# Kernel tuning notes

Measured on AMD Instinct MI355X. Metric: run time of the kernel, lower is better.

## Reference

```python
import jax, jax.numpy as jnp
import numpy as np

D_MODEL = 1024
N_HEAD = 16
D_K = D_MODEL // N_HEAD
MAX_LEN = 1000
LN_EPS = 1e-5


def setup_inputs() -> dict:
    key = jax.random.key(0)
    ks = jax.random.split(key, 12)
    B, S = 4, 1000
    def xavier(k, shape):
        fan_in, fan_out = shape[1], shape[0]
        lim = np.sqrt(6.0 / (fan_in + fan_out))
        return jax.random.uniform(k, shape, jnp.float32, -lim, lim)
    return {
        "q": jax.random.normal(ks[0], (B, S, D_MODEL), jnp.float32),
        "k": jax.random.normal(ks[1], (B, S, D_MODEL), jnp.float32),
        "v": jax.random.normal(ks[2], (B, S, D_MODEL), jnp.float32),
        "ln_g": jnp.ones((D_MODEL,), jnp.float32),
        "ln_b": jnp.zeros((D_MODEL,), jnp.float32),
        "wq": xavier(ks[3], (D_MODEL, D_MODEL)),
        "bq": jnp.zeros((D_MODEL,), jnp.float32),
        "wk": xavier(ks[4], (D_MODEL, D_MODEL)),
        "bk": jnp.zeros((D_MODEL,), jnp.float32),
        "wv": xavier(ks[5], (D_MODEL, D_MODEL)),
        "bv": jnp.zeros((D_MODEL,), jnp.float32),
        "wo": xavier(ks[6], (D_MODEL, D_MODEL)),
        "bo": jnp.zeros((D_MODEL,), jnp.float32),
        "rel_emb": jax.random.normal(ks[7], (2 * MAX_LEN - 1, D_K), jnp.float32) / np.sqrt(D_K),
    }


def _layer_norm(x, g, b):
    mu = jnp.mean(x, axis=-1, keepdims=True)
    var = jnp.mean(jnp.square(x - mu), axis=-1, keepdims=True)
    return (x - mu) * jax.lax.rsqrt(var + LN_EPS) * g + b


def reference(q, k, v, ln_g, ln_b, wq, bq, wk, bk, wv, bv, wo, bo, rel_emb):
    B, S, _ = q.shape
    residual = q
    qn = _layer_norm(q, ln_g, ln_b)
    kn = _layer_norm(k, ln_g, ln_b)
    vn = _layer_norm(v, ln_g, ln_b)
    # torch Linear: y = x @ W^T + b; reshape to [B, H, S, d_k]
    def proj(x, w, b):
        return (x @ w.T + b).reshape(B, S, N_HEAD, D_K).transpose(0, 2, 1, 3)
    qh = proj(qn, wq, bq)
    kh = proj(kn, wk, bk)
    vh = proj(vn, wv, bv)
    scale = 1.0 / np.sqrt(D_K)
    scores = jnp.einsum('bhid,bhjd->bhij', qh, kh) * scale
    # relative position bias: rel_pos[i, j] = emb[center + (i - j)]
    center = MAX_LEN - 1
    start = center - (S - 1)
    window = jax.lax.dynamic_slice_in_dim(rel_emb, start, 2 * S - 1, axis=0)  # [2S-1, d_k]
    pos = jnp.arange(S)
    rel_idx = pos[:, None] - pos[None, :] + (S - 1)  # [S, S] in [0, 2S-2]
    rel_pos = window[rel_idx]  # [S, S, d_k]
    scores = scores + jnp.einsum('bhik,ijk->bhij', qh, rel_pos) * scale
    attn = jax.nn.softmax(scores, axis=-1)
    out = jnp.einsum('bhij,bhjd->bhid', attn, vh)
    out = out.transpose(0, 2, 1, 3).reshape(B, S, D_MODEL)
    out = out @ wo.T + bo
    return out + residual
```

## Files before the change

kernel.cpp:

```cpp
#include <hip/hip_runtime.h>
#include <hip/hip_bf16.h>

#define D_MODEL 1024
#define N_HEAD  16
#define D_K     64
#define MAX_LEN 1000
#define B_      4
#define S_      1000
#define S_PAD   1024
#define M_PAD   (B_ * S_PAD)
#define M_REAL  (B_ * S_)
#define LN_EPS  1e-5f
#define SCALE_L2E 0.1803368801111204f
#define REL_ROWS (2*MAX_LEN-1)

typedef __attribute__((ext_vector_type(8))) short short8;
typedef __attribute__((ext_vector_type(4))) float f32x4;

__device__ __forceinline__ unsigned short f2b(float f) {
    unsigned u = __builtin_bit_cast(unsigned, f);
    u = (u + 0x7FFFu + ((u >> 16) & 1u)) >> 16;
    return (unsigned short)u;
}

__device__ __forceinline__ unsigned short f2b_trunc(float f) {
    return (unsigned short)(__builtin_bit_cast(unsigned, f) >> 16);
}

__device__ __forceinline__ float b2f(unsigned short u) {
    return __builtin_bit_cast(float, (unsigned)u << 16);
}

__device__ __forceinline__ f32x4 mfma16(short8 a, short8 b, f32x4 c) {
    return __builtin_amdgcn_mfma_f32_16x16x32_bf16(a, b, c, 0, 0, 0);
}

__device__ __forceinline__ void gload_lds16(const void* g, void* l) {
    __builtin_amdgcn_global_load_lds(
        (const __attribute__((address_space(1))) unsigned int*)g,
        (__attribute__((address_space(3))) unsigned int*)l, 16, 0, 0);
}

#define DPPROR(x, S) __builtin_bit_cast(float, __builtin_amdgcn_update_dpp( \
        0, __builtin_bit_cast(int, (x)), 0x120 | (S), 0xF, 0xF, false))

__global__ void prep_all(const float* __restrict__ wq, const float* __restrict__ wk,
                         const float* __restrict__ wv, const float* __restrict__ wo,
                         const float* __restrict__ rel,
                         unsigned short* __restrict__ wqb, unsigned short* __restrict__ wkb,
                         unsigned short* __restrict__ wvb, unsigned short* __restrict__ wob,
                         unsigned short* __restrict__ relb,
                         const float* __restrict__ xq, const float* __restrict__ xk,
                         const float* __restrict__ xv, const float* __restrict__ g,
                         const float* __restrict__ beta,
                         unsigned short* __restrict__ yq, unsigned short* __restrict__ yk,
                         unsigned short* __restrict__ yv) {
    __shared__ float rs[4], rq[4];
    int bid = blockIdx.x;
    int tid = threadIdx.x;
    if (bid < 5120) {
        int y = bid >> 10;
        const float* in; unsigned short* out; int n4;
        switch (y) {
            case 0: in = wq; out = wqb; n4 = 262144; break;
            case 1: in = wk; out = wkb; n4 = 262144; break;
            case 2: in = wv; out = wvb; n4 = 262144; break;
            case 3: in = wo; out = wob; n4 = 262144; break;
            default: in = rel; out = relb; n4 = REL_ROWS * D_K / 4; break;
        }
        int i = (bid & 1023) * 256 + tid;
        if (i >= n4) return;
        float4 v = ((const float4*)in)[i];
        ushort4 o;
        o.x = f2b(v.x); o.y = f2b(v.y); o.z = f2b(v.z); o.w = f2b(v.w);
        ((ushort4*)out)[i] = o;
        return;
    }
    int r2 = bid - 5120;
    int which = r2 >> 12;
    int r = r2 & 4095;
    const float* x = which == 0 ? xq : which == 1 ? xk : xv;
    unsigned short* y = which == 0 ? yq : which == 1 ? yk : yv;
    int b = r >> 10, i = r & 1023;
    unsigned short* yr = y + (size_t)r * D_MODEL;
    if (i >= S_) {
#pragma unroll
        for (int l = 0; l < 4; ++l) yr[tid + l * 256] = 0;
        return;
    }
    const float* xr = x + ((size_t)b * S_ + i) * D_MODEL;
    float v[4];
    float s = 0.f, sq = 0.f;
#pragma unroll
    for (int l = 0; l < 4; ++l) {
        v[l] = xr[tid + l * 256];
        s += v[l];
        sq += v[l] * v[l];
    }
#pragma unroll
    for (int o = 32; o > 0; o >>= 1) {
        s += __shfl_down(s, o, 64);
        sq += __shfl_down(sq, o, 64);
    }
    if ((tid & 63) == 0) { rs[tid >> 6] = s; rq[tid >> 6] = sq; }
    __syncthreads();
    if (tid == 0) {
        rs[0] = rs[0] + rs[1] + rs[2] + rs[3];
        rq[0] = rq[0] + rq[1] + rq[2] + rq[3];
    }
    __syncthreads();
    float mu = rs[0] * (1.0f / D_MODEL);
    float var = rq[0] * (1.0f / D_MODEL) - mu * mu;
    float rstd = rsqrtf(var + LN_EPS);
#pragma unroll
    for (int l = 0; l < 4; ++l) {
        int c = tid + l * 256;
        yr[c] = f2b((v[l] - mu) * rstd * g[c] + beta[c]);
    }
}

template<int MODE>
__device__ __forceinline__ void gemm_body(
        const unsigned short* __restrict__ X, const unsigned short* __restrict__ W,
        const float* __restrict__ bias, const float* __restrict__ resid,
        unsigned short* __restrict__ Yb, float* __restrict__ Yf,
        unsigned short* As, unsigned short* Bs, int row0, int col0) {
    int tid = threadIdx.x;
    int lane = tid & 63, w = tid >> 6;
    int wr = w >> 1, wc = w & 1;
    int fr = lane & 15, fk = (lane >> 4) * 8;

    f32x4 acc[4][4];
#pragma unroll
    for (int fm = 0; fm < 4; ++fm)
#pragma unroll
        for (int fn = 0; fn < 4; ++fn) acc[fm][fn] = (f32x4)0.f;

    int c0 = (w * 2 + 0) * 64 + lane;
    int c1 = (w * 2 + 1) * 64 + lane;
    const unsigned short* xs0 = X + (size_t)(row0 + (c0 >> 2)) * 1024 + (c0 & 3) * 8;
    const unsigned short* xs1 = X + (size_t)(row0 + (c1 >> 2)) * 1024 + (c1 & 3) * 8;
    const unsigned short* ws0 = W + (size_t)(col0 + (c0 >> 2)) * 1024 + (c0 & 3) * 8;
    const unsigned short* ws1 = W + (size_t)(col0 + (c1 >> 2)) * 1024 + (c1 & 3) * 8;
    int do0 = (w * 2 + 0) * 512;
    int do1 = (w * 2 + 1) * 512;

    auto stage = [&](int buf, int k0) {
        gload_lds16(xs0 + k0, As + buf * 4096 + do0);
        gload_lds16(xs1 + k0, As + buf * 4096 + do1);
        gload_lds16(ws0 + k0, Bs + buf * 4096 + do0);
        gload_lds16(ws1 + k0, Bs + buf * 4096 + do1);
    };

    stage(0, 0);

    for (int it = 0; it < 32; ++it) {
        __syncthreads();
        if (it < 31) stage((it & 1) ^ 1, (it + 1) * 32);

        const unsigned short* Ab = As + (it & 1) * 4096;
        const unsigned short* Bb = Bs + (it & 1) * 4096;
        short8 a[4], b[4];
#pragma unroll
        for (int fm = 0; fm < 4; ++fm)
            a[fm] = *(const short8*)(Ab + (wr * 64 + fm * 16 + fr) * 32 + fk);
#pragma unroll
        for (int fn = 0; fn < 4; ++fn)
            b[fn] = *(const short8*)(Bb + (wc * 64 + fn * 16 + fr) * 32 + fk);
#pragma unroll
        for (int fm = 0; fm < 4; ++fm)
#pragma unroll
            for (int fn = 0; fn < 4; ++fn)
                acc[fm][fn] = mfma16(a[fm], b[fn], acc[fm][fn]);
    }

#pragma unroll
    for (int fm = 0; fm < 4; ++fm) {
#pragma unroll
        for (int fn = 0; fn < 4; ++fn) {
            int cg = col0 + wc * 64 + fn * 16 + fr;
            float bv = bias[cg];
#pragma unroll
            for (int r = 0; r < 4; ++r) {
                int rg = row0 + wr * 64 + fm * 16 + (lane >> 4) * 4 + r;
                float val = acc[fm][fn][r] + bv;
                int b_ = rg >> 10, i = rg & 1023;
                if (MODE == 0) {
                    int h = cg >> 6, d = cg & 63;
                    Yb[(((size_t)(b_ * N_HEAD + h)) * S_PAD + i) * D_K + d] = f2b(val);
                } else if (MODE == 1) {
                    int h = cg >> 6, d = cg & 63;
                    Yb[(((size_t)(b_ * N_HEAD + h)) * D_K + d) * S_PAD + i] = f2b(val);
                } else {
                    if (i < S_) {
                        size_t orow = (size_t)b_ * S_ + i;
                        Yf[orow * 1024 + cg] = val + resid[orow * 1024 + cg];
                    }
                }
            }
        }
    }
}

__global__ __launch_bounds__(256) void gemm_qkv(
        const unsigned short* __restrict__ qn, const unsigned short* __restrict__ kn,
        const unsigned short* __restrict__ vn,
        const unsigned short* __restrict__ wqb, const unsigned short* __restrict__ wkb,
        const unsigned short* __restrict__ wvb,
        const float* __restrict__ bq, const float* __restrict__ bk,
        const float* __restrict__ bv,
        unsigned short* __restrict__ qh, unsigned short* __restrict__ kh,
        unsigned short* __restrict__ vt) {
    __shared__ __align__(16) unsigned short As[2][128 * 32];
    __shared__ __align__(16) unsigned short Bs[2][128 * 32];
    int fid = blockIdx.x + (blockIdx.y << 3) + (blockIdx.z << 8);
    int swz = (fid & 7) * 96 + (fid >> 3);
    int bz = swz >> 8;
    int rem = swz & 255;
    int row0 = (rem >> 3) * 128, col0 = (rem & 7) * 128;
    if (bz == 0)
        gemm_body<0>(qn, wqb, bq, nullptr, qh, nullptr, As[0], Bs[0], row0, col0);
    else if (bz == 1)
        gemm_body<0>(kn, wkb, bk, nullptr, kh, nullptr, As[0], Bs[0], row0, col0);
    else
        gemm_body<1>(vn, wvb, bv, nullptr, vt, nullptr, As[0], Bs[0], row0, col0);
}

__global__ __launch_bounds__(256) void gemm_out(
        const unsigned short* __restrict__ X, const unsigned short* __restrict__ W,
        const float* __restrict__ bias, const float* __restrict__ resid,
        float* __restrict__ Yf) {
    __shared__ __align__(16) unsigned short As[2][128 * 32];
    __shared__ __align__(16) unsigned short Bs[2][128 * 32];
    int fid = blockIdx.x + (blockIdx.y << 3);
    int swz = (fid & 7) * 32 + (fid >> 3);
    int row0 = (swz >> 3) * 128, col0 = (swz & 7) * 128;
    gemm_body<2>(X, W, bias, resid, nullptr, Yf, As[0], Bs[0], row0, col0);
}

#define QRT 20
#define QPW 1600
#define PW  72
__device__ __forceinline__ void attn_slab(
        const unsigned short* __restrict__ Kc, const unsigned short* __restrict__ Vc,
        unsigned short* __restrict__ qp, const short8 (*rl)[2],
        short8 aq0, short8 aq1, f32x4* accO, float* mrun, float* lrun,
        bool mask_needed, int j0, int fr, int fk8, int rgrp, int rsw) {
    f32x4 accS[4];
#pragma unroll
    for (int fj = 0; fj < 4; ++fj) accS[fj] = (f32x4)0.f;
    __builtin_amdgcn_s_setprio(1);
#pragma unroll
    for (int fj = 0; fj < 4; ++fj) {
        int kb = (fj * 16 + fr) * 64 + fk8;
        accS[fj] = mfma16(aq0, *(const short8*)(Kc + (kb ^ rsw)), accS[fj]);
        accS[fj] = mfma16(aq1, *(const short8*)(Kc + ((kb + 32) ^ rsw)), accS[fj]);
    }
#pragma unroll
    for (int fu = 0; fu < 5; ++fu) {
        f32x4 qr = (f32x4)0.f;
        qr = mfma16(aq0, rl[fu][0], qr);
        qr = mfma16(aq1, rl[fu][1], qr);
        unsigned lo = ((unsigned)f2b_trunc(qr[1]) << 16) | f2b_trunc(qr[0]);
        unsigned hi = ((unsigned)f2b_trunc(qr[3]) << 16) | f2b_trunc(qr[2]);
        *(uint2*)(qp + (fu * 16 + fr) * QRT + rgrp) = uint2{lo, hi};
    }
    __builtin_amdgcn_s_setprio(0);

    float sc[4][4];
#pragma unroll
    for (int fj = 0; fj < 4; ++fj) {
        int j_loc = fj * 16 + fr;
#pragma unroll
        for (int r = 0; r < 4; ++r) {
            int col = rgrp + r - j_loc + 63;
            sc[fj][r] = (accS[fj][r] + b2f(qp[col * QRT + rgrp + r])) * SCALE_L2E;
        }
    }
    if (mask_needed) {
#pragma unroll
        for (int fj = 0; fj < 4; ++fj) {
            int j_loc = fj * 16 + fr;
            if (j0 + j_loc >= S_) {
#pragma unroll
                for (int r = 0; r < 4; ++r) sc[fj][r] = -3e38f;
            }
        }
    }

    float pm[4];
#pragma unroll
    for (int r = 0; r < 4; ++r) {
        float m0 = fmaxf(fmaxf(sc[0][r], sc[1][r]), fmaxf(sc[2][r], sc[3][r]));
        m0 = fmaxf(m0, DPPROR(m0, 1));
        m0 = fmaxf(m0, DPPROR(m0, 2));
        m0 = fmaxf(m0, DPPROR(m0, 4));
        m0 = fmaxf(m0, DPPROR(m0, 8));
        pm[r] = m0;
    }

    float dmax = fmaxf(fmaxf(pm[0] - mrun[0], pm[1] - mrun[1]),
                       fmaxf(pm[2] - mrun[2], pm[3] - mrun[3]));
    if (!__all(dmax <= 8.0f)) {
#pragma unroll
        for (int r = 0; r < 4; ++r) {
            float mn = fmaxf(mrun[r], pm[r]);
            float scl = __builtin_amdgcn_exp2f(mrun[r] - mn);
            mrun[r] = mn;
            lrun[r] *= scl;
#pragma unroll
            for (int fd = 0; fd < 4; ++fd) accO[fd][r] *= scl;
        }
    }

    float rsum[4];
#pragma unroll
    for (int r = 0; r < 4; ++r) rsum[r] = 0.f;
#pragma unroll
    for (int fj = 0; fj < 4; ++fj) {
#pragma unroll
        for (int r = 0; r < 4; ++r) {
            float p = __builtin_amdgcn_exp2f(sc[fj][r] - mrun[r]);
            rsum[r] += p;
            qp[(rgrp + r) * PW + fj * 16 + fr] = f2b_trunc(p);
        }
    }
#pragma unroll
    for (int r = 0; r < 4; ++r) {
        float s0 = rsum[r];
        s0 += DPPROR(s0, 1);
        s0 += DPPROR(s0, 2);
        s0 += DPPROR(s0, 4);
        s0 += DPPROR(s0, 8);
        lrun[r] += s0;
    }

    short8 ap0 = *(const short8*)(qp + fr * PW + fk8);
    short8 ap1 = *(const short8*)(qp + fr * PW + 32 + fk8);
    __builtin_amdgcn_s_setprio(1);
#pragma unroll
    for (int fd = 0; fd < 4; ++fd) {
        int vb = (fd * 16 + fr) * 64 + fk8;
        accO[fd] = mfma16(ap0, *(const short8*)(Vc + (vb ^ rsw)), accO[fd]);
        accO[fd] = mfma16(ap1, *(const short8*)(Vc + ((vb + 32) ^ rsw)), accO[fd]);
    }
    __builtin_amdgcn_s_setprio(0);
}

__global__ __launch_bounds__(256, 2) void attn_mfma(
        const unsigned short* __restrict__ qh, const unsigned short* __restrict__ kh,
        const unsigned short* __restrict__ vt, const unsigned short* __restrict__ relb,
        unsigned short* __restrict__ aout) {
    __shared__ __align__(16) unsigned short Ks[2][64 * 64];
    __shared__ __align__(16) unsigned short Vs[2][64 * 64];
    __shared__ __align__(16) unsigned short QP[8][QPW];

    int tid = threadIdx.x, lane = tid & 63, w = tid >> 6;
    int bid = blockIdx.x;
    int swz = (bid & 7) * 64 + (bid >> 3);
    int bh = swz >> 3;
    int i0a = (((swz & 7) * 8) + 2 * w) * 16;
    int fr = lane & 15, fk8 = (lane >> 4) * 8, rgrp = (lane >> 4) * 4;
    int rsw = (fr & 7) << 3;

    const unsigned short* kbase = kh + (size_t)bh * S_PAD * D_K;
    const unsigned short* vtbase = vt + (size_t)bh * D_K * S_PAD;

    const unsigned short* qpa = qh + ((size_t)bh * S_PAD + i0a + fr) * D_K + fk8;
    short8 aqa0 = *(const short8*)(qpa);
    short8 aqa1 = *(const short8*)(qpa + 32);
    const unsigned short* qpb = qpa + 16 * D_K;
    short8 aqb0 = *(const short8*)(qpb);
    short8 aqb1 = *(const short8*)(qpb + 32);

    f32x4 accOa[4], accOb[4];
    float mruna[4], lruna[4], mrunb[4], lrunb[4];
#pragma unroll
    for (int fd = 0; fd < 4; ++fd) { accOa[fd] = (f32x4)0.f; accOb[fd] = (f32x4)0.f; }
#pragma unroll
    for (int r = 0; r < 4; ++r) {
        mruna[r] = -3e38f; lruna[r] = 0.f;
        mrunb[r] = -3e38f; lrunb[r] = 0.f;
    }

    unsigned short* qpA = QP[w];
    unsigned short* qpB = QP[4 + w];
    int row_in = lane >> 3, slot = lane & 7;

    auto stage = [&](int buf, int it2) {
        int j0s = it2 * 64;
#pragma unroll
        for (int cc = 0; cc < 2; ++cc) {
            int c = w * 2 + cc;
            int r = c * 8 + row_in;
            gload_lds16(kbase + (size_t)(j0s + r) * 64 + (slot ^ row_in) * 8,
                        &Ks[buf][c * 512]);
        }
#pragma unroll
        for (int cc = 0; cc < 2; ++cc) {
            int c = w * 2 + cc;
            int d = c * 8 + row_in;
            gload_lds16(vtbase + (size_t)d * S_PAD + j0s + (slot ^ row_in) * 8,
                        &Vs[buf][c * 512]);
        }
    };

    stage(0, 0);
    __syncthreads();

    for (int it = 0; it < 16; ++it) {
        int cur = it & 1, j0 = it * 64;
        bool mask_needed = (j0 + 63 >= S_);

        short8 rl[6][2];
        int ub = i0a - j0 + (S_ - D_K);
#pragma unroll
        for (int fu = 0; fu < 6; ++fu) {
            int u = ub + fu * 16 + fr;
            u = u < 0 ? 0 : (u > REL_ROWS - 1 ? REL_ROWS - 1 : u);
            const unsigned short* rp = relb + (size_t)u * D_K + fk8;
            rl[fu][0] = *(const short8*)(rp);
            rl[fu][1] = *(const short8*)(rp + 32);
        }
        __builtin_amdgcn_sched_barrier(0);

        if (it < 15) stage(cur ^ 1, it + 1);

        attn_slab(Ks[cur], Vs[cur], qpA, rl, aqa0, aqa1, accOa, mruna, lruna,
                  mask_needed, j0, fr, fk8, rgrp, rsw);
        attn_slab(Ks[cur], Vs[cur], qpB, rl + 1, aqb0, aqb1, accOb, mrunb, lrunb,
                  mask_needed, j0, fr, fk8, rgrp, rsw);

        __syncthreads();
    }

    int b_ = bh >> 4, h = bh & 15;
#pragma unroll
    for (int r = 0; r < 4; ++r) {
        float inva = 1.0f / lruna[r];
        float invb = 1.0f / lrunb[r];
        int ma = b_ * S_PAD + i0a + rgrp + r;
        int mb = ma + 16;
#pragma unroll
        for (int fd = 0; fd < 4; ++fd) {
            int c = h * D_K + fd * 16 + fr;
            aout[(size_t)ma * D_MODEL + c] = f2b(accOa[fd][r] * inva);
            aout[(size_t)mb * D_MODEL + c] = f2b(accOb[fd][r] * invb);
        }
    }
}

extern "C" void kernel_launch(void* const* d_in, const int* in_sizes, int n_in,
                              void* d_out, int out_size, void* d_ws, size_t ws_size,
                              hipStream_t stream) {
    const float* q    = (const float*)d_in[0];
    const float* k    = (const float*)d_in[1];
    const float* v    = (const float*)d_in[2];
    const float* ln_g = (const float*)d_in[3];
    const float* ln_b = (const float*)d_in[4];
    const float* wq   = (const float*)d_in[5];
    const float* bq   = (const float*)d_in[6];
    const float* wk   = (const float*)d_in[7];
    const float* bk   = (const float*)d_in[8];
    const float* wv   = (const float*)d_in[9];
    const float* bv   = (const float*)d_in[10];
    const float* wo   = (const float*)d_in[11];
    const float* bo   = (const float*)d_in[12];
    const float* rel  = (const float*)d_in[13];
    float* out = (float*)d_out;

    const size_t TSZ = (size_t)M_PAD * D_MODEL;
    unsigned short* ws   = (unsigned short*)d_ws;
    unsigned short* qn   = ws;
    unsigned short* kn   = qn + TSZ;
    unsigned short* vn   = kn + TSZ;
    unsigned short* qh   = vn + TSZ;
    unsigned short* kh   = qh + TSZ;
    unsigned short* vt   = kh + TSZ;
    unsigned short* aout = vt + TSZ;
    unsigned short* wqb  = aout + TSZ;
    unsigned short* wkb  = wqb + 1024 * 1024;
    unsigned short* wvb  = wkb + 1024 * 1024;
    unsigned short* wob  = wvb + 1024 * 1024;
    unsigned short* relb = wob + 1024 * 1024;

    prep_all<<<5120 + 3 * 4096, 256, 0, stream>>>(
        wq, wk, wv, wo, rel, wqb, wkb, wvb, wob, relb,
        q, k, v, ln_g, ln_b, qn, kn, vn);

    gemm_qkv<<<dim3(8, 32, 3), 256, 0, stream>>>(qn, kn, vn, wqb, wkb, wvb,
                                                 bq, bk, bv, qh, kh, vt);

    attn_mfma<<<512, 256, 0, stream>>>(qh, kh, vt, relb, aout);

    gemm_out<<<dim3(8, 32), 256, 0, stream>>>(aout, wob, bo, q, out);
}
```

Baseline: 166.0 us.

## Interleave two query slabs per wave and fold softmax scale into Q projection

The two per-wave query slabs, previously processed one after the other, are now handled together in one routine. Each K and V fragment read from LDS feeds both slabs' MFMAs, and the independent softmax chains interleave for more instruction-level parallelism. The softmax scale times log2(e) is now applied once in the Q projection epilogue, which removes the per-score multiply in attention. The cost is higher register pressure under the two-blocks-per-CU launch bound, plus a small precision change because the scaled Q is rounded to bf16.

Result: no change. 163.6 us (median of 2 runs) (-1.4%).

```diff
diff --git a/kernel.cpp b/kernel.cpp
--- a/kernel.cpp
+++ b/kernel.cpp
@@ -185,7 +185,8 @@
                 int rg = row0 + wr * 64 + fm * 16 + (lane >> 4) * 4 + r;
                 float val = acc[fm][fn][r] + bv;
                 int b_ = rg >> 10, i = rg & 1023;
-                if (MODE == 0) {
+                if (MODE == 0 || MODE == 3) {
+                    if (MODE == 3) val *= SCALE_L2E;
                     int h = cg >> 6, d = cg & 63;
                     Yb[(((size_t)(b_ * N_HEAD + h)) * S_PAD + i) * D_K + d] = f2b(val);
                 } else if (MODE == 1) {
@@ -219,7 +220,7 @@
     int rem = swz & 255;
     int row0 = (rem >> 3) * 128, col0 = (rem & 7) * 128;
     if (bz == 0)
-        gemm_body<0>(qn, wqb, bq, nullptr, qh, nullptr, As[0], Bs[0], row0, col0);
+        gemm_body<3>(qn, wqb, bq, nullptr, qh, nullptr, As[0], Bs[0], row0, col0);
     else if (bz == 1)
         gemm_body<0>(kn, wkb, bk, nullptr, kh, nullptr, As[0], Bs[0], row0, col0);
     else
@@ -241,40 +242,57 @@
 #define QRT 20
 #define QPW 1600
 #define PW  72
-__device__ __forceinline__ void attn_slab(
+__device__ __forceinline__ void attn_pair(
         const unsigned short* __restrict__ Kc, const unsigned short* __restrict__ Vc,
-        unsigned short* __restrict__ qp, const short8 (*rl)[2],
-        short8 aq0, short8 aq1, f32x4* accO, float* mrun, float* lrun,
+        unsigned short* __restrict__ qpA, unsigned short* __restrict__ qpB,
+        const short8 (*rl)[2],
+        short8 aqa0, short8 aqa1, short8 aqb0, short8 aqb1,
+        f32x4* accOa, f32x4* accOb,
+        float* mra, float* lra, float* mrb, float* lrb,
         bool mask_needed, int j0, int fr, int fk8, int rgrp, int rsw) {
-    f32x4 accS[4];
-#pragma unroll
-    for (int fj = 0; fj < 4; ++fj) accS[fj] = (f32x4)0.f;
+    f32x4 accS0[4], accS1[4];
+#pragma unroll
+    for (int fj = 0; fj < 4; ++fj) { accS0[fj] = (f32x4)0.f; accS1[fj] = (f32x4)0.f; }
     __builtin_amdgcn_s_setprio(1);
 #pragma unroll
     for (int fj = 0; fj < 4; ++fj) {
         int kb = (fj * 16 + fr) * 64 + fk8;
-        accS[fj] = mfma16(aq0, *(const short8*)(Kc + (kb ^ rsw)), accS[fj]);
-        accS[fj] = mfma16(aq1, *(const short8*)(Kc + ((kb + 32) ^ rsw)), accS[fj]);
+        short8 kf0 = *(const short8*)(Kc + (kb ^ rsw));
+        short8 kf1 = *(const short8*)(Kc + ((kb + 32) ^ rsw));
+        accS0[fj] = mfma16(aqa0, kf0, accS0[fj]);
+        accS1[fj] = mfma16(aqb0, kf0, accS1[fj]);
+        accS0[fj] = mfma16(aqa1, kf1, accS0[fj]);
+        accS1[fj] = mfma16(aqb1, kf1, accS1[fj]);
     }
 #pragma unroll
     for (int fu = 0; fu < 5; ++fu) {
         f32x4 qr = (f32x4)0.f;
-        qr = mfma16(aq0, rl[fu][0], qr);
-        qr = mfma16(aq1, rl[fu][1], qr);
+        qr = mfma16(aqa0, rl[fu][0], qr);
+        qr = mfma16(aqa1, rl[fu][1], qr);
         unsigned lo = ((unsigned)f2b_trunc(qr[1]) << 16) | f2b_trunc(qr[0]);
         unsigned hi = ((unsigned)f2b_trunc(qr[3]) << 16) | f2b_trunc(qr[2]);
-        *(uint2*)(qp + (fu * 16 + fr) * QRT + rgrp) = uint2{lo, hi};
+        *(uint2*)(qpA + (fu * 16 + fr) * QRT + rgrp) = uint2{lo, hi};
+    }
+#pragma unroll
+    for (int fu = 0; fu < 5; ++fu) {
+        f32x4 qr = (f32x4)0.f;
+        qr = mfma16(aqb0, rl[fu + 1][0], qr);
+        qr = mfma16(aqb1, rl[fu + 1][1], qr);
+        unsigned lo = ((unsigned)f2b_trunc(qr[1]) << 16) | f2b_trunc(qr[0]);
+        unsigned hi = ((unsigned)f2b_trunc(qr[3]) << 16) | f2b_trunc(qr[2]);
+        *(uint2*)(qpB + (fu * 16 + fr) * QRT + rgrp) = uint2{lo, hi};
     }
     __builtin_amdgcn_s_setprio(0);
 
-    float sc[4][4];
+    float sc0[4][4], sc1[4][4];
 #pragma unroll
     for (int fj = 0; fj < 4; ++fj) {
         int j_loc = fj * 16 + fr;
 #pragma unroll
         for (int r = 0; r < 4; ++r) {
             int col = rgrp + r - j_loc + 63;
-            sc[fj][r] = (accS[fj][r] + b2f(qp[col * QRT + rgrp + r])) * SCALE_L2E;
+            sc0[fj][r] = accS0[fj][r] + b2f(qpA[col * QRT + rgrp + r]);
+            sc1[fj][r] = accS1[fj][r] + b2f(qpB[col * QRT + rgrp + r]);
         }
     }
     if (mask_needed) {
@@ -283,66 +301,88 @@
             int j_loc = fj * 16 + fr;
             if (j0 + j_loc >= S_) {
 #pragma unroll
-                for (int r = 0; r < 4; ++r) sc[fj][r] = -3e38f;
+                for (int r = 0; r < 4; ++r) { sc0[fj][r] = -3e38f; sc1[fj][r] = -3e38f; }
             }
         }
     }
 
-    float pm[4];
+    float pma[4], pmb[4];
 #pragma unroll
     for (int r = 0; r < 4; ++r) {
-        float m0 = fmaxf(fmaxf(sc[0][r], sc[1][r]), fmaxf(sc[2][r], sc[3][r]));
-        m0 = fmaxf(m0, DPPROR(m0, 1));
-        m0 = fmaxf(m0, DPPROR(m0, 2));
-        m0 = fmaxf(m0, DPPROR(m0, 4));
-        m0 = fmaxf(m0, DPPROR(m0, 8));
-        pm[r] = m0;
-    }
-
-    float dmax = fmaxf(fmaxf(pm[0] - mrun[0], pm[1] - mrun[1]),
-                       fmaxf(pm[2] - mrun[2], pm[3] - mrun[3]));
-    if (!__all(dmax <= 8.0f)) {
+        float m0 = fmaxf(fmaxf(sc0[0][r], sc0[1][r]), fmaxf(sc0[2][r], sc0[3][r]));
+        float m1 = fmaxf(fmaxf(sc1[0][r], sc1[1][r]), fmaxf(sc1[2][r], sc1[3][r]));
+        m0 = fmaxf(m0, DPPROR(m0, 1)); m1 = fmaxf(m1, DPPROR(m1, 1));
+        m0 = fmaxf(m0, DPPROR(m0, 2)); m1 = fmaxf(m1, DPPROR(m1, 2));
+        m0 = fmaxf(m0, DPPROR(m0, 4)); m1 = fmaxf(m1, DPPROR(m1, 4));
+        m0 = fmaxf(m0, DPPROR(m0, 8)); m1 = fmaxf(m1, DPPROR(m1, 8));
+        pma[r] = m0; pmb[r] = m1;
+    }
+
+    float dmaxa = fmaxf(fmaxf(pma[0] - mra[0], pma[1] - mra[1]),
+                        fmaxf(pma[2] - mra[2], pma[3] - mra[3]));
+    if (!__all(dmaxa <= 8.0f)) {
 #pragma unroll
         for (int r = 0; r < 4; ++r) {
-            float mn = fmaxf(mrun[r], pm[r]);
-            float scl = __builtin_amdgcn_exp2f(mrun[r] - mn);
-            mrun[r] = mn;
-            lrun[r] *= scl;
-#pragma unroll
-            for (int fd = 0; fd < 4; ++fd) accO[fd][r] *= scl;
-        }
-    }
-
-    float rsum[4];
-#pragma unroll
-    for (int r = 0; r < 4; ++r) rsum[r] = 0.f;
+            float mn = fmaxf(mra[r], pma[r]);
+            float scl = __builtin_amdgcn_exp2f(mra[r] - mn);
+            mra[r] = mn;
+            lra[r] *= scl;
+#pragma unroll
+            for (int fd = 0; fd < 4; ++fd) accOa[fd][r] *= scl;
+        }
+    }
+    float dmaxb = fmaxf(fmaxf(pmb[0] - mrb[0], pmb[1] - mrb[1]),
+                        fmaxf(pmb[2] - mrb[2], pmb[3] - mrb[3]));
+    if (!__all(dmaxb <= 8.0f)) {
+#pragma unroll
+        for (int r = 0; r < 4; ++r) {
+            float mn = fmaxf(mrb[r], pmb[r]);
+            float scl = __builtin_amdgcn_exp2f(mrb[r] - mn);
+            mrb[r] = mn;
+            lrb[r] *= scl;
+#pragma unroll
+            for (int fd = 0; fd < 4; ++fd) accOb[fd][r] *= scl;
+        }
+    }
+
+    float rsa[4], rsb[4];
+#pragma unroll
+    for (int r = 0; r < 4; ++r) { rsa[r] = 0.f; rsb[r] = 0.f; }
 #pragma unroll
     for (int fj = 0; fj < 4; ++fj) {
 #pragma unroll
         for (int r = 0; r < 4; ++r) {
-            float p = __builtin_amdgcn_exp2f(sc[fj][r] - mrun[r]);
-            rsum[r] += p;
-            qp[(rgrp + r) * PW + fj * 16 + fr] = f2b_trunc(p);
+            float p0 = __builtin_amdgcn_exp2f(sc0[fj][r] - mra[r]);
+            float p1 = __builtin_amdgcn_exp2f(sc1[fj][r] - mrb[r]);
+            rsa[r] += p0; rsb[r] += p1;
+            qpA[(rgrp + r) * PW + fj * 16 + fr] = f2b_trunc(p0);
+            qpB[(rgrp + r) * PW + fj * 16 + fr] = f2b_trunc(p1);
         }
     }
 #pragma unroll
     for (int r = 0; r < 4; ++r) {
-        float s0 = rsum[r];
-        s0 += DPPROR(s0, 1);
-        s0 += DPPROR(s0, 2);
-        s0 += DPPROR(s0, 4);
-        s0 += DPPROR(s0, 8);
-        lrun[r] += s0;
-    }
-
-    short8 ap0 = *(const short8*)(qp + fr * PW + fk8);
-    short8 ap1 = *(const short8*)(qp + fr * PW + 32 + fk8);
+        float s0 = rsa[r], s1 = rsb[r];
+        s0 += DPPROR(s0, 1); s1 += DPPROR(s1, 1);
+        s0 += DPPROR(s0, 2); s1 += DPPROR(s1, 2);
+        s0 += DPPROR(s0, 4); s1 += DPPROR(s1, 4);
+        s0 += DPPROR(s0, 8); s1 += DPPROR(s1, 8);
+        lra[r] += s0; lrb[r] += s1;
+    }
+
+    short8 apA0 = *(const short8*)(qpA + fr * PW + fk8);
+    short8 apA1 = *(const short8*)(qpA + fr * PW + 32 + fk8);
+    short8 apB0 = *(const short8*)(qpB + fr * PW + fk8);
+    short8 apB1 = *(const short8*)(qpB + fr * PW + 32 + fk8);
     __builtin_amdgcn_s_setprio(1);
 #pragma unroll
     for (int fd = 0; fd < 4; ++fd) {
         int vb = (fd * 16 + fr) * 64 + fk8;
-        accO[fd] = mfma16(ap0, *(const short8*)(Vc + (vb ^ rsw)), accO[fd]);
-        accO[fd] = mfma16(ap1, *(const short8*)(Vc + ((vb + 32) ^ rsw)), accO[fd]);
+        short8 vf0 = *(const short8*)(Vc + (vb ^ rsw));
+        short8 vf1 = *(const short8*)(Vc + ((vb + 32) ^ rsw));
+        accOa[fd] = mfma16(apA0, vf0, accOa[fd]);
+        accOb[fd] = mfma16(apB0, vf0, accOb[fd]);
+        accOa[fd] = mfma16(apA1, vf1, accOa[fd]);
+        accOb[fd] = mfma16(apB1, vf1, accOb[fd]);
     }
     __builtin_amdgcn_s_setprio(0);
 }
@@ -426,9 +466,9 @@
 
         if (it < 15) stage(cur ^ 1, it + 1);
 
-        attn_slab(Ks[cur], Vs[cur], qpA, rl, aqa0, aqa1, accOa, mruna, lruna,
-                  mask_needed, j0, fr, fk8, rgrp, rsw);
-        attn_slab(Ks[cur], Vs[cur], qpB, rl + 1, aqb0, aqb1, accOb, mrunb, lrunb,
+        attn_pair(Ks[cur], Vs[cur], qpA, qpB, rl,
+                  aqa0, aqa1, aqb0, aqb1, accOa, accOb,
+                  mruna, lruna, mrunb, lrunb,
                   mask_needed, j0, fr, fk8, rgrp, rsw);
 
         __syncthreads();
```
